# Kernel optimization log

Measured on AMD Instinct MI355X. Metric: run time of the kernel, lower is better.

Reference implementation:

```python
import jax, jax.numpy as jnp
import numpy as np

B = 65536          # batch
N_IN = 256         # input nodes (topology level 0)
G = 16             # node groups per level (joined nodes with shared dependency set)
U = 16             # units (joined nodes) per group -> 256 nodes per level
F = 32             # fan-in (input_node_coords) per group
LEVELS = 4


def setup_inputs() -> dict:
    key = jax.random.key(0)
    ks = jax.random.split(key, 13)
    inp = {"x": jax.random.normal(ks[0], (B, N_IN), dtype=jnp.float32)}
    for l in range(LEVELS):
        inp[f"k{l+1}"] = jax.random.normal(ks[1 + 3 * l], (G, F, U), dtype=jnp.float32) * 0.2
        inp[f"b{l+1}"] = jax.random.normal(ks[2 + 3 * l], (G, U), dtype=jnp.float32) * 0.1
        # flat coords into concatenation of all prior level outputs (levels 0..l)
        hi = N_IN + l * (G * U)
        inp[f"idx{l+1}"] = jax.random.randint(ks[3 + 3 * l], (G, F), 0, hi, dtype=jnp.int32)
    return inp


def reference(x, k1, b1, k2, b2, k3, b3, k4, b4, idx1, idx2, idx3, idx4):
    kernels = [k1, k2, k3, k4]
    biases = [b1, b2, b3, b4]
    idxs = [idx1, idx2, idx3, idx4]
    # `flat` is the column-wise concatenation of all prior topology-level outputs
    # (equivalent to the `inputs` list of per-level tensors in the original model,
    # with (layer_index, node_index) coords flattened to a single column index).
    flat = x
    out = x
    for K, b, idx in zip(kernels, biases, idxs):
        sel = flat[:, idx]                                   # gather: [B, G, F]
        out = jnp.tanh(jnp.einsum('bgf,gfu->bgu', sel, K) + b)  # tiny matmul+bias+act
        out = out.reshape(out.shape[0], G * U)               # per-level concat of groups
        flat = jnp.concatenate([flat, out], axis=1)
    return out  # last level output, [B, G*U]
```

## Files before the change

kernel.cpp:

```cpp
#include <hip/hip_runtime.h>
#include <stdint.h>

#define NIN 256
#define RPB 32

typedef float    f32x4 __attribute__((ext_vector_type(4)));
typedef _Float16 half8 __attribute__((ext_vector_type(8)));
typedef __fp16   fp16x2 __attribute__((ext_vector_type(2)));
typedef uint32_t u32x4 __attribute__((ext_vector_type(4)));

#define SEL_LO 0x05040100u
#define SEL_HI 0x07060302u

static __device__ __forceinline__ float fast_tanh(float x) {
    float e = __builtin_amdgcn_exp2f(x * 2.8853900817779268f);
    return 1.0f - 2.0f * __builtin_amdgcn_rcpf(e + 1.0f);
}
static __device__ __forceinline__ unsigned pkrtz(float a, float b) {
    fp16x2 h = __builtin_amdgcn_cvt_pkrtz(a, b);
    return __builtin_bit_cast(unsigned, h);
}

extern "C" __global__ void kprep_kernel(const float* __restrict__ k1, const float* __restrict__ k2,
                                        const float* __restrict__ k3, const float* __restrict__ k4,
                                        const int* __restrict__ i1, const int* __restrict__ i2,
                                        const int* __restrict__ i3, const int* __restrict__ i4,
                                        uint32_t* __restrict__ kt, int* __restrict__ apre) {
    const int bx  = blockIdx.x;
    const int lvl = bx >> 2;
    const float* Kp = (lvl == 0) ? k1 : (lvl == 1) ? k2 : (lvl == 2) ? k3 : k4;
    const int*   Ip = (lvl == 0) ? i1 : (lvl == 1) ? i2 : (lvl == 2) ? i3 : i4;
    const int sub = (bx & 3) * 256 + threadIdx.x;
    const int g = sub >> 6, q = (sub >> 4) & 3, n = sub & 15;
    const float* src = Kp + (size_t)(g * 32 + q * 8) * 16 + n;
    const float v0 = src[0],  v1 = src[16], v2 = src[32], v3 = src[48];
    const float v4 = src[64], v5 = src[80], v6 = src[96], v7 = src[112];
    u32x4 pk;
    pk.x = pkrtz(v0, v1); pk.y = pkrtz(v2, v3);
    pk.z = pkrtz(v4, v5); pk.w = pkrtz(v6, v7);
    *(u32x4*)(kt + (size_t)(lvl * 1024 + sub) * 4) = pk;

    if ((bx & 3) < 2) {
        const int f = (bx & 3) * 256 + threadIdx.x;
        const int col = Ip[f];
        apre[lvl * 512 + f] = (col << 6) ^ (((col >> 1) & 3) << 4);
    }
}


extern "C" __global__ __launch_bounds__(512, 4)
void denc_kernel(const float* __restrict__ x,
                 const int* __restrict__ a1, const float* __restrict__ b1,
                 const int* __restrict__ a2, const float* __restrict__ b2,
                 const int* __restrict__ a3, const float* __restrict__ b3,
                 const int* __restrict__ a4, const float* __restrict__ b4,
                 const uint32_t* __restrict__ kt,
                 float* __restrict__ out)
{
    __shared__ int4 ftile[4096];
    const char* tfc = (const char*)ftile;

    const int tid  = threadIdx.x;
    const int w    = tid >> 6;
    const int lane = tid & 63;
    const int q    = lane >> 4;
    const int n    = lane & 15;
    const int gbase = w * 2;
    const int R0   = blockIdx.x * RPB;
    const int Ln   = n << 2;

    {
        const int c  = tid & 255;
        const int ph = (tid >> 8) * 8;
        const float* xb = x + (size_t)R0 * 256 + c;
        uint32_t qp[8];
        #pragma unroll
        for (int j = 0; j < 8; ++j) {
            const float t0 = xb[(size_t)(ph + j) * 256];
            const float t1 = xb[(size_t)(ph + j + 16) * 256];
            qp[j] = pkrtz(t0, t1);
        }
        const int s = (c >> 1) & 3;
        ftile[c * 4 + ((ph >> 2) ^ s)]     = make_int4(qp[0], qp[1], qp[2], qp[3]);
        ftile[c * 4 + (((ph >> 2) + 1) ^ s)] = make_int4(qp[4], qp[5], qp[6], qp[7]);
    }

#define LEVEL(Ap, Bp, LVLBASE, OB, LAST) do { \
    __syncthreads(); \
    _Pragma("unroll") \
    for (int gi = 0; gi < 2; ++gi) { \
        const int gg = gbase + gi; \
        const u32x4 bf = *(const u32x4*)(kt + (size_t)((LVLBASE) + gg * 64 + q * 16 + n) * 4); \
        const float bvv = (Bp)[gg * 16 + n]; \
        f32x4 accA = {bvv, bvv, bvv, bvv}, accB = accA; \
        const int4 pa = *(const int4*)((Ap) + gg * 32 + q * 8); \
        const int4 pb = *(const int4*)((Ap) + gg * 32 + q * 8 + 4); \
        const uint32_t r0 = *(const uint32_t*)(tfc + (pa.x ^ Ln)); \
        const uint32_t r1 = *(const uint32_t*)(tfc + (pa.y ^ Ln)); \
        const uint32_t r2 = *(const uint32_t*)(tfc + (pa.z ^ Ln)); \
        const uint32_t r3 = *(const uint32_t*)(tfc + (pa.w ^ Ln)); \
        const uint32_t r4 = *(const uint32_t*)(tfc + (pb.x ^ Ln)); \
        const uint32_t r5 = *(const uint32_t*)(tfc + (pb.y ^ Ln)); \
        const uint32_t r6 = *(const uint32_t*)(tfc + (pb.z ^ Ln)); \
        const uint32_t r7 = *(const uint32_t*)(tfc + (pb.w ^ Ln)); \
        u32x4 fA, fB; \
        fA.x = __builtin_amdgcn_perm(r1, r0, SEL_LO); fB.x = __builtin_amdgcn_perm(r1, r0, SEL_HI); \
        fA.y = __builtin_amdgcn_perm(r3, r2, SEL_LO); fB.y = __builtin_amdgcn_perm(r3, r2, SEL_HI); \
        fA.z = __builtin_amdgcn_perm(r5, r4, SEL_LO); fB.z = __builtin_amdgcn_perm(r5, r4, SEL_HI); \
        fA.w = __builtin_amdgcn_perm(r7, r6, SEL_LO); fB.w = __builtin_amdgcn_perm(r7, r6, SEL_HI); \
        accA = __builtin_amdgcn_mfma_f32_16x16x32_f16( \
            __builtin_bit_cast(half8, fA), __builtin_bit_cast(half8, bf), accA, 0, 0, 0); \
        accB = __builtin_amdgcn_mfma_f32_16x16x32_f16( \
            __builtin_bit_cast(half8, fB), __builtin_bit_cast(half8, bf), accB, 0, 0, 0); \
        const float tA0 = fast_tanh(accA[0]), tA1 = fast_tanh(accA[1]); \
        const float tA2 = fast_tanh(accA[2]), tA3 = fast_tanh(accA[3]); \
        const float tB0 = fast_tanh(accB[0]), tB1 = fast_tanh(accB[1]); \
        const float tB2 = fast_tanh(accB[2]), tB3 = fast_tanh(accB[3]); \
        if (LAST) { \
            float* ob = out + (size_t)(R0 + q * 4) * 256 + gg * 16 + n; \
            ob[0]    = tA0; ob[256]  = tA1; ob[512]  = tA2; ob[768]  = tA3; \
            ob[4096] = tB0; ob[4352] = tB1; ob[4608] = tB2; ob[4864] = tB3; \
        } else { \
            const int col = (OB) + gg * 16 + n; \
            const int s = (col >> 1) & 3; \
            ftile[col * 4 + (q ^ s)] = make_int4( \
                pkrtz(tA0, tB0), pkrtz(tA1, tB1), pkrtz(tA2, tB2), pkrtz(tA3, tB3)); \
        } \
    } \
} while (0)

    LEVEL(a1, b1,    0, NIN,       0);
    LEVEL(a2, b2, 1024, NIN + 256, 0);
    LEVEL(a3, b3, 2048, NIN + 512, 0);
    LEVEL(a4, b4, 3072, 0,         1);

#undef LEVEL
}

extern "C" void kernel_launch(void* const* d_in, const int* in_sizes, int n_in,
                              void* d_out, int out_size, void* d_ws, size_t ws_size,
                              hipStream_t stream) {
    const float* x  = (const float*)d_in[0];
    const float* k1 = (const float*)d_in[1];
    const float* b1 = (const float*)d_in[2];
    const int*   i1 = (const int*)  d_in[3];
    const float* k2 = (const float*)d_in[4];
    const float* b2 = (const float*)d_in[5];
    const int*   i2 = (const int*)  d_in[6];
    const float* k3 = (const float*)d_in[7];
    const float* b3 = (const float*)d_in[8];
    const int*   i3 = (const int*)  d_in[9];
    const float* k4 = (const float*)d_in[10];
    const float* b4 = (const float*)d_in[11];
    const int*   i4 = (const int*)  d_in[12];
    float* out = (float*)d_out;
    uint32_t* kt = (uint32_t*)d_ws;
    int* apre = (int*)((char*)d_ws + 65536);

    hipLaunchKernelGGL(kprep_kernel, dim3(16), dim3(256), 0, stream,
                       k1, k2, k3, k4, i1, i2, i3, i4, kt, apre);

    const int batch = in_sizes[0] / NIN;
    hipLaunchKernelGGL(denc_kernel, dim3(batch / RPB), dim3(512), 0, stream,
                       x, apre, b1, apre + 512, b2, apre + 1024, b3, apre + 1536, b4,
                       (const uint32_t*)kt, out);
}
```

Baseline: 44.29 us.

## Use 1024-thread blocks with one group per wave and prefetch next-level indices

Doubles the block to 16 waves so each wave handles a single node group per level rather than two, and splits the x staging load across four thread slices. It also loads the next level's gather indices before the current level's MFMA work, taking that load off the critical path after each barrier. The cost is larger blocks, a __syncthreads across 16 waves per level, and tighter per-thread register limits from the new launch bounds.

```diff
diff --git a/kernel.cpp b/kernel.cpp
--- a/kernel.cpp
+++ b/kernel.cpp
@@ -48,7 +48,7 @@
 }
 
 
-extern "C" __global__ __launch_bounds__(512, 4)
+extern "C" __global__ __launch_bounds__(1024, 8)
 void denc_kernel(const float* __restrict__ x,
                  const int* __restrict__ a1, const float* __restrict__ b1,
                  const int* __restrict__ a2, const float* __restrict__ b2,
@@ -65,73 +65,72 @@
     const int lane = tid & 63;
     const int q    = lane >> 4;
     const int n    = lane & 15;
-    const int gbase = w * 2;
     const int R0   = blockIdx.x * RPB;
     const int Ln   = n << 2;
 
     {
-        const int c  = tid & 255;
-        const int ph = (tid >> 8) * 8;
+        const int c = tid & 255;
+        const int j = tid >> 8;
         const float* xb = x + (size_t)R0 * 256 + c;
-        uint32_t qp[8];
+        uint32_t qp[4];
         #pragma unroll
-        for (int j = 0; j < 8; ++j) {
-            const float t0 = xb[(size_t)(ph + j) * 256];
-            const float t1 = xb[(size_t)(ph + j + 16) * 256];
-            qp[j] = pkrtz(t0, t1);
+        for (int k = 0; k < 4; ++k) {
+            const int p = j * 4 + k;
+            qp[k] = pkrtz(xb[(size_t)p * 256], xb[(size_t)(p + 16) * 256]);
         }
         const int s = (c >> 1) & 3;
-        ftile[c * 4 + ((ph >> 2) ^ s)]     = make_int4(qp[0], qp[1], qp[2], qp[3]);
-        ftile[c * 4 + (((ph >> 2) + 1) ^ s)] = make_int4(qp[4], qp[5], qp[6], qp[7]);
+        ftile[c * 4 + (j ^ s)] = make_int4((int)qp[0], (int)qp[1], (int)qp[2], (int)qp[3]);
     }
 
-#define LEVEL(Ap, Bp, LVLBASE, OB, LAST) do { \
+    int4 pa = *(const int4*)(a1 + w * 32 + q * 8);
+    int4 pb = *(const int4*)(a1 + w * 32 + q * 8 + 4);
+
+#define LEVEL(ApNext, Bp, LVLBASE, OB, LAST) do { \
     __syncthreads(); \
-    _Pragma("unroll") \
-    for (int gi = 0; gi < 2; ++gi) { \
-        const int gg = gbase + gi; \
-        const u32x4 bf = *(const u32x4*)(kt + (size_t)((LVLBASE) + gg * 64 + q * 16 + n) * 4); \
-        const float bvv = (Bp)[gg * 16 + n]; \
-        f32x4 accA = {bvv, bvv, bvv, bvv}, accB = accA; \
-        const int4 pa = *(const int4*)((Ap) + gg * 32 + q * 8); \
-        const int4 pb = *(const int4*)((Ap) + gg * 32 + q * 8 + 4); \
-        const uint32_t r0 = *(const uint32_t*)(tfc + (pa.x ^ Ln)); \
-        const uint32_t r1 = *(const uint32_t*)(tfc + (pa.y ^ Ln)); \
-        const uint32_t r2 = *(const uint32_t*)(tfc + (pa.z ^ Ln)); \
-        const uint32_t r3 = *(const uint32_t*)(tfc + (pa.w ^ Ln)); \
-        const uint32_t r4 = *(const uint32_t*)(tfc + (pb.x ^ Ln)); \
-        const uint32_t r5 = *(const uint32_t*)(tfc + (pb.y ^ Ln)); \
-        const uint32_t r6 = *(const uint32_t*)(tfc + (pb.z ^ Ln)); \
-        const uint32_t r7 = *(const uint32_t*)(tfc + (pb.w ^ Ln)); \
-        u32x4 fA, fB; \
-        fA.x = __builtin_amdgcn_perm(r1, r0, SEL_LO); fB.x = __builtin_amdgcn_perm(r1, r0, SEL_HI); \
-        fA.y = __builtin_amdgcn_perm(r3, r2, SEL_LO); fB.y = __builtin_amdgcn_perm(r3, r2, SEL_HI); \
-        fA.z = __builtin_amdgcn_perm(r5, r4, SEL_LO); fB.z = __builtin_amdgcn_perm(r5, r4, SEL_HI); \
-        fA.w = __builtin_amdgcn_perm(r7, r6, SEL_LO); fB.w = __builtin_amdgcn_perm(r7, r6, SEL_HI); \
-        accA = __builtin_amdgcn_mfma_f32_16x16x32_f16( \
-            __builtin_bit_cast(half8, fA), __builtin_bit_cast(half8, bf), accA, 0, 0, 0); \
-        accB = __builtin_amdgcn_mfma_f32_16x16x32_f16( \
-            __builtin_bit_cast(half8, fB), __builtin_bit_cast(half8, bf), accB, 0, 0, 0); \
-        const float tA0 = fast_tanh(accA[0]), tA1 = fast_tanh(accA[1]); \
-        const float tA2 = fast_tanh(accA[2]), tA3 = fast_tanh(accA[3]); \
-        const float tB0 = fast_tanh(accB[0]), tB1 = fast_tanh(accB[1]); \
-        const float tB2 = fast_tanh(accB[2]), tB3 = fast_tanh(accB[3]); \
-        if (LAST) { \
-            float* ob = out + (size_t)(R0 + q * 4) * 256 + gg * 16 + n; \
-            ob[0]    = tA0; ob[256]  = tA1; ob[512]  = tA2; ob[768]  = tA3; \
-            ob[4096] = tB0; ob[4352] = tB1; ob[4608] = tB2; ob[4864] = tB3; \
-        } else { \
-            const int col = (OB) + gg * 16 + n; \
-            const int s = (col >> 1) & 3; \
-            ftile[col * 4 + (q ^ s)] = make_int4( \
-                pkrtz(tA0, tB0), pkrtz(tA1, tB1), pkrtz(tA2, tB2), pkrtz(tA3, tB3)); \
-        } \
+    const uint32_t r0 = *(const uint32_t*)(tfc + (pa.x ^ Ln)); \
+    const uint32_t r1 = *(const uint32_t*)(tfc + (pa.y ^ Ln)); \
+    const uint32_t r2 = *(const uint32_t*)(tfc + (pa.z ^ Ln)); \
+    const uint32_t r3 = *(const uint32_t*)(tfc + (pa.w ^ Ln)); \
+    const uint32_t r4 = *(const uint32_t*)(tfc + (pb.x ^ Ln)); \
+    const uint32_t r5 = *(const uint32_t*)(tfc + (pb.y ^ Ln)); \
+    const uint32_t r6 = *(const uint32_t*)(tfc + (pb.z ^ Ln)); \
+    const uint32_t r7 = *(const uint32_t*)(tfc + (pb.w ^ Ln)); \
+    if (!(LAST)) {                                    \
+        pa = *(const int4*)((ApNext) + w * 32 + q * 8); \
+        pb = *(const int4*)((ApNext) + w * 32 + q * 8 + 4); \
+    } \
+    const u32x4 bf = *(const u32x4*)(kt + (size_t)((LVLBASE) + w * 64 + q * 16 + n) * 4); \
+    const float bvv = (Bp)[w * 16 + n]; \
+    f32x4 accA = {bvv, bvv, bvv, bvv}, accB = accA; \
+    u32x4 fA, fB; \
+    fA.x = __builtin_amdgcn_perm(r1, r0, SEL_LO); fB.x = __builtin_amdgcn_perm(r1, r0, SEL_HI); \
+    fA.y = __builtin_amdgcn_perm(r3, r2, SEL_LO); fB.y = __builtin_amdgcn_perm(r3, r2, SEL_HI); \
+    fA.z = __builtin_amdgcn_perm(r5, r4, SEL_LO); fB.z = __builtin_amdgcn_perm(r5, r4, SEL_HI); \
+    fA.w = __builtin_amdgcn_perm(r7, r6, SEL_LO); fB.w = __builtin_amdgcn_perm(r7, r6, SEL_HI); \
+    accA = __builtin_amdgcn_mfma_f32_16x16x32_f16( \
+        __builtin_bit_cast(half8, fA), __builtin_bit_cast(half8, bf), accA, 0, 0, 0); \
+    accB = __builtin_amdgcn_mfma_f32_16x16x32_f16( \
+        __builtin_bit_cast(half8, fB), __builtin_bit_cast(half8, bf), accB, 0, 0, 0); \
+    const float tA0 = fast_tanh(accA[0]), tA1 = fast_tanh(accA[1]); \
+    const float tA2 = fast_tanh(accA[2]), tA3 = fast_tanh(accA[3]); \
+    const float tB0 = fast_tanh(accB[0]), tB1 = fast_tanh(accB[1]); \
+    const float tB2 = fast_tanh(accB[2]), tB3 = fast_tanh(accB[3]); \
+    if (LAST) { \
+        float* ob = out + (size_t)(R0 + q * 4) * 256 + w * 16 + n; \
+        ob[0]    = tA0; ob[256]  = tA1; ob[512]  = tA2; ob[768]  = tA3; \
+        ob[4096] = tB0; ob[4352] = tB1; ob[4608] = tB2; ob[4864] = tB3; \
+    } else { \
+        const int col = (OB) + w * 16 + n; \
+        const int s = (col >> 1) & 3; \
+        ftile[col * 4 + (q ^ s)] = make_int4( \
+            (int)pkrtz(tA0, tB0), (int)pkrtz(tA1, tB1), \
+            (int)pkrtz(tA2, tB2), (int)pkrtz(tA3, tB3)); \
     } \
 } while (0)
 
-    LEVEL(a1, b1,    0, NIN,       0);
-    LEVEL(a2, b2, 1024, NIN + 256, 0);
-    LEVEL(a3, b3, 2048, NIN + 512, 0);
+    LEVEL(a2, b1,    0, NIN,       0);
+    LEVEL(a3, b2, 1024, NIN + 256, 0);
+    LEVEL(a4, b3, 2048, NIN + 512, 0);
     LEVEL(a4, b4, 3072, 0,         1);
 
 #undef LEVEL
@@ -161,7 +160,7 @@
                        k1, k2, k3, k4, i1, i2, i3, i4, kt, apre);
 
     const int batch = in_sizes[0] / NIN;
-    hipLaunchKernelGGL(denc_kernel, dim3(batch / RPB), dim3(512), 0, stream,
+    hipLaunchKernelGGL(denc_kernel, dim3(batch / RPB), dim3(1024), 0, stream,
                        x, apre, b1, apre + 512, b2, apre + 1024, b3, apre + 1536, b4,
                        (const uint32_t*)kt, out);
 }
```

After: 40.83 us. 1.08x faster.
